# Kernel tuning notes

Hardware: AMD Instinct MI355X
Metric: run time of the kernel (lower is better)

Reference implementation:

```python
import jax, jax.numpy as jnp
import numpy as np

POSE, Z, H, E = 62, 32, 256, 6

def setup_inputs() -> dict:
    key = jax.random.key(0)
    ks = jax.random.split(key, 32)
    it = iter(ks)
    def W(o, i):
        return (jax.random.normal(next(it), (o, i), jnp.float32) * 0.05)
    def B(o):
        return jnp.zeros((o,), jnp.float32)
    def WE(o, i):
        return (jax.random.normal(next(it), (E, o, i), jnp.float32) * 0.05)
    def BE(o):
        return jnp.zeros((E, o), jnp.float32)
    d = {}
    d['prev_pose'] = jax.random.normal(next(it), (POSE,), jnp.float32)
    d['curr_pose'] = jax.random.normal(next(it), (POSE,), jnp.float32)
    d['eps'] = jax.random.normal(next(it), (Z,), jnp.float32)
    # encoder
    d['enc_w0'], d['enc_b0'] = W(H, POSE + POSE), B(H)
    d['enc_w1'], d['enc_b1'] = W(H, H), B(H)
    d['enc_w2'], d['enc_b2'] = W(H, H), B(H)
    d['mu_w'], d['mu_b'] = W(Z, H), B(Z)
    d['lv_w'], d['lv_b'] = W(Z, H), B(Z)
    # gating network
    d['gate_w0'], d['gate_b0'] = W(H, Z + POSE), B(H)
    d['gate_w1'], d['gate_b1'] = W(H, H), B(H)
    d['gate_w2'], d['gate_b2'] = W(H, H), B(H)
    d['gate_w3'], d['gate_b3'] = W(E, H), B(E)
    # 6 experts, stacked on leading expert axis
    d['exp_w0'], d['exp_b0'] = WE(H, Z + POSE), BE(H)
    d['exp_w1'], d['exp_b1'] = WE(H, Z + H), BE(H)
    d['exp_w2'], d['exp_b2'] = WE(H, Z + H), BE(H)
    d['exp_w3'], d['exp_b3'] = WE(POSE, Z + H), BE(POSE)
    return d

def _forward(prev_pose, curr_pose, eps,
             enc_w0, enc_b0, enc_w1, enc_b1, enc_w2, enc_b2,
             mu_w, mu_b, lv_w, lv_b,
             gate_w0, gate_b0, gate_w1, gate_b1, gate_w2, gate_b2,
             gate_w3, gate_b3,
             exp_w0, exp_b0, exp_w1, exp_b1, exp_w2, exp_b2,
             exp_w3, exp_b3):
    elu = jax.nn.elu
    # encode
    x = elu(enc_w0 @ jnp.concatenate([prev_pose, curr_pose]) + enc_b0)
    x = elu(enc_w1 @ x + enc_b1)
    x = elu(enc_w2 @ x + enc_b2)
    mu = mu_w @ x + mu_b
    logvar = lv_w @ x + lv_b
    # reparameterize (eps supplied as input for determinism)
    z = mu + eps * jnp.exp(0.5 * logvar)
    # gating network (raw logits, no softmax -- as in the original)
    g_in = jnp.concatenate([z, prev_pose])  # [94]
    g = elu(gate_w0 @ g_in + gate_b0)
    g = elu(gate_w1 @ g + gate_b1)
    g = elu(gate_w2 @ g + gate_b2)
    gates = gate_w3 @ g + gate_b3  # [6]
    # all 6 experts batched along leading axis e
    z_e = jnp.broadcast_to(z, (E, Z))  # [6,32]
    h = elu(jnp.einsum('eoh,h->eo', exp_w0, g_in) + exp_b0)       # [6,256]
    h = elu(jnp.einsum('eoh,eh->eo', exp_w1,
                       jnp.concatenate([z_e, h], axis=1)) + exp_b1)
    h = elu(jnp.einsum('eoh,eh->eo', exp_w2,
                       jnp.concatenate([z_e, h], axis=1)) + exp_b2)
    out_e = jnp.einsum('eoh,eh->eo', exp_w3,
                       jnp.concatenate([z_e, h], axis=1)) + exp_b3  # [6,62]
    decoded = jnp.sum(out_e * gates[:, None], axis=0)  # [62]
    return decoded, mu, logvar

def reference(prev_pose, curr_pose, eps,
              enc_w0, enc_b0, enc_w1, enc_b1, enc_w2, enc_b2,
              mu_w, mu_b, lv_w, lv_b,
              gate_w0, gate_b0, gate_w1, gate_b1, gate_w2, gate_b2,
              gate_w3, gate_b3,
              exp_w0, exp_b0, exp_w1, exp_b1, exp_w2, exp_b2,
              exp_w3, exp_b3):
    return _forward(prev_pose, curr_pose, eps,
                    enc_w0, enc_b0, enc_w1, enc_b1, enc_w2, enc_b2,
                    mu_w, mu_b, lv_w, lv_b,
                    gate_w0, gate_b0, gate_w1, gate_b1, gate_w2, gate_b2,
                    gate_w3, gate_b3,
                    exp_w0, exp_b0, exp_w1, exp_b1, exp_w2, exp_b2,
                    exp_w3, exp_b3)
```

## Files before the change

kernel.cpp:

```cpp
#include <hip/hip_runtime.h>
#include <math.h>


#define NWG   256
#define BLOCK 256

__device__ __align__(128) float g_a0[256];
__device__ __align__(128) float g_a1[256];
__device__ __align__(128) float g_a2[256];
__device__ __align__(128) float g_mu[32];
__device__ __align__(128) float g_lv[32];
__device__ __align__(128) float g_g0[256];
__device__ __align__(128) float g_g1[256];
__device__ __align__(128) float g_g2[256];
__device__ __align__(128) float g_gates[32];
__device__ __align__(128) float g_h0[1536];
__device__ __align__(128) float g_h1[1536];
__device__ __align__(128) float g_h2[1536];
__device__ __align__(128) float g_oute[384];

struct P {
  const float *prev, *curr, *eps;
  const float *ew0,*eb0,*ew1,*eb1,*ew2,*eb2;
  const float *muw,*mub,*lvw,*lvb;
  const float *gw0,*gb0,*gw1,*gb1,*gw2,*gb2,*gw3,*gb3;
  const float *xw0,*xb0,*xw1,*xb1,*xw2,*xb2,*xw3,*xb3;
  float* out;
};

__device__ __forceinline__ float cload(const float* a) {
  int v = __hip_atomic_load((const int*)a, __ATOMIC_RELAXED,
                            __HIP_MEMORY_SCOPE_AGENT);
  return __int_as_float(v);
}
__device__ __forceinline__ void cstore(float* a, float v) {
  __hip_atomic_store((int*)a, __float_as_int(v), __ATOMIC_RELAXED,
                     __HIP_MEMORY_SCOPE_AGENT);
}
__device__ __forceinline__ float4 cload4(const float* a) {
  float4 r;
  r.x = cload(a + 0); r.y = cload(a + 1);
  r.z = cload(a + 2); r.w = cload(a + 3);
  return r;
}
__device__ __forceinline__ float wred(float v) {
#pragma unroll
  for (int m = 32; m; m >>= 1) v += __shfl_xor(v, m, 64);
  return v;
}
__device__ __forceinline__ float elu(float x) { return x > 0.f ? x : expm1f(x); }
__device__ __forceinline__ float dot4(float4 a, float4 b) {
  return a.x*b.x + a.y*b.y + a.z*b.z + a.w*b.w;
}

__device__ __forceinline__ void gridbar(int* flags, int phase) {
  __syncthreads();
  if (threadIdx.x == 0)
    __hip_atomic_store(&flags[blockIdx.x * 16], phase,
                       __ATOMIC_RELAXED, __HIP_MEMORY_SCOPE_AGENT);
  if (threadIdx.x < 64) {
    const int l = threadIdx.x;
    for (;;) {
      int v0 = __hip_atomic_load(&flags[(l)       * 16], __ATOMIC_RELAXED, __HIP_MEMORY_SCOPE_AGENT);
      int v1 = __hip_atomic_load(&flags[(l +  64) * 16], __ATOMIC_RELAXED, __HIP_MEMORY_SCOPE_AGENT);
      int v2 = __hip_atomic_load(&flags[(l + 128) * 16], __ATOMIC_RELAXED, __HIP_MEMORY_SCOPE_AGENT);
      int v3 = __hip_atomic_load(&flags[(l + 192) * 16], __ATOMIC_RELAXED, __HIP_MEMORY_SCOPE_AGENT);
      if (min(min(v0, v1), min(v2, v3)) >= phase) break;
      __builtin_amdgcn_s_sleep(2);
    }
  }
  __syncthreads();
}

__device__ __forceinline__ void row288(const float* wr, float b,
                                       float4 z4, const float* hsrc,
                                       float* dst, bool doelu, int lane) {
  float4 w = *(const float4*)(wr + 4 * lane);
  float we = (lane < 32) ? wr[256 + lane] : 0.f;
  float4 xh = z4;
  if (lane >= 8) xh = cload4(hsrc + 4 * lane - 32);
  float s = dot4(w, xh);
  if (lane < 32) s += we * cload(hsrc + 224 + lane);
  s = wred(s);
  if (!lane) cstore(dst, doelu ? elu(s + b) : (s + b));
}

__device__ __forceinline__ void row256(const float* wr, float b,
                                       const float* xsrc, float* dst,
                                       bool doelu, int lane) {
  float4 w = *(const float4*)(wr + 4 * lane);
  float4 x = cload4(xsrc + 4 * lane);
  float s = wred(dot4(w, x));
  if (!lane) cstore(dst, doelu ? elu(s + b) : (s + b));
}

__global__ __launch_bounds__(BLOCK, 1) void mvae_main(P p, int* flags) {
  const int tid  = threadIdx.x;
  const int lane = tid & 63;
  const int wvin = tid >> 6;
  const int Wv   = blockIdx.x * 4 + wvin;

  __shared__ float s_o[384];
  __shared__ float s_gg[8];

  if (Wv < 256) {
    const float* wr = p.ew0 + Wv * 124;
    float wa = wr[lane];
    float wb = (lane < 60) ? wr[64 + lane] : 0.f;
    float xa = (lane < 62) ? p.prev[lane] : p.curr[lane - 62];
    float xb = (lane < 60) ? p.curr[lane + 2] : 0.f;
    float s = wred(wa * xa + wb * xb);
    if (!lane) cstore(&g_a0[Wv], elu(s + p.eb0[Wv]));
  }
  gridbar(flags, 1);

  if (Wv < 256)
    row256(p.ew1 + Wv * 256, p.eb1[Wv], g_a0, &g_a1[Wv], true, lane);
  gridbar(flags, 2);

  if (Wv < 256)
    row256(p.ew2 + Wv * 256, p.eb2[Wv], g_a1, &g_a2[Wv], true, lane);
  gridbar(flags, 3);

  if (Wv < 64) {
    const float* wr = (Wv < 32) ? p.muw + Wv * 256 : p.lvw + (Wv - 32) * 256;
    float4 w = *(const float4*)(wr + 4 * lane);
    float4 x = cload4(g_a2 + 4 * lane);
    float s = wred(dot4(w, x));
    if (!lane) {
      if (Wv < 32) { float v = s + p.mub[Wv]; cstore(&g_mu[Wv], v); p.out[62 + Wv] = v; }
      else { int r = Wv - 32; float v = s + p.lvb[r]; cstore(&g_lv[r], v); p.out[94 + r] = v; }
    }
  }
  gridbar(flags, 4);

  float zs = 0.f;
  if (lane < 32)
    zs = cload(&g_mu[lane]) + p.eps[lane] * expf(0.5f * cload(&g_lv[lane]));
  float4 z4;
  z4.x = __shfl(zs, (4 * lane + 0) & 63, 64);
  z4.y = __shfl(zs, (4 * lane + 1) & 63, 64);
  z4.z = __shfl(zs, (4 * lane + 2) & 63, 64);
  z4.w = __shfl(zs, (4 * lane + 3) & 63, 64);
  float prevA = (lane >= 32 && lane < 94) ? p.prev[lane - 32] : 0.f;
  float prevB = (lane < 30) ? p.prev[32 + lane] : 0.f;
  float xa94 = (lane < 32) ? zs : prevA;

  {
#pragma unroll
    for (int k = 0; k < 2; ++k) {
      int r = Wv + 1024 * k;
      if (r < 1792) {
        const float* wr = (r < 256) ? p.gw0 + r * 94 : p.xw0 + (size_t)(r - 256) * 94;
        float wa = wr[lane];
        float wb = (lane < 30) ? wr[64 + lane] : 0.f;
        float s = wred(wa * xa94 + wb * prevB);
        if (!lane) {
          if (r < 256) cstore(&g_g0[r], elu(s + p.gb0[r]));
          else         cstore(&g_h0[r - 256], elu(s + p.xb0[r - 256]));
        }
      }
    }
  }
  gridbar(flags, 5);

  {
#pragma unroll
    for (int k = 0; k < 2; ++k) {
      int r = Wv + 1024 * k;
      if (r < 1792) {
        if (r < 256)
          row256(p.gw1 + r * 256, p.gb1[r], g_g0, &g_g1[r], true, lane);
        else {
          int q = r - 256, e = q >> 8;
          row288(p.xw1 + (size_t)q * 288, p.xb1[q], z4, g_h0 + e * 256,
                 &g_h1[q], true, lane);
        }
      }
    }
  }
  gridbar(flags, 6);

  {
#pragma unroll
    for (int k = 0; k < 2; ++k) {
      int r = Wv + 1024 * k;
      if (r < 1792) {
        if (r < 256)
          row256(p.gw2 + r * 256, p.gb2[r], g_g1, &g_g2[r], true, lane);
        else {
          int q = r - 256, e = q >> 8;
          row288(p.xw2 + (size_t)q * 288, p.xb2[q], z4, g_h1 + e * 256,
                 &g_h2[q], true, lane);
        }
      }
    }
  }
  gridbar(flags, 7);

  if (Wv < 6) {
    row256(p.gw3 + Wv * 256, p.gb3[Wv], g_g2, &g_gates[Wv], false, lane);
  } else if (Wv < 378) {
    int q = Wv - 6, e = q / 62;
    row288(p.xw3 + (size_t)q * 288, p.xb3[q], z4, g_h2 + e * 256,
           &g_oute[q], false, lane);
  }
  gridbar(flags, 8);

  if (blockIdx.x == 0) {
    s_o[tid] = cload(&g_oute[tid]);
    if (tid < 116) s_o[tid + 256] = cload(&g_oute[tid + 256]);
    if (tid < 6)   s_gg[tid] = cload(&g_gates[tid]);
    __syncthreads();
    if (tid < 62) {
      float s = 0.f;
#pragma unroll
      for (int e = 0; e < 6; ++e) s += s_o[e * 62 + tid] * s_gg[e];
      p.out[tid] = s;
    }
  }
}

extern "C" void kernel_launch(void* const* d_in, const int* in_sizes, int n_in,
                              void* d_out, int out_size, void* d_ws, size_t ws_size,
                              hipStream_t stream) {
  (void)in_sizes; (void)n_in; (void)out_size; (void)ws_size;
  const float* const* in = (const float* const*)d_in;
  P p;
  p.prev = in[0];  p.curr = in[1];  p.eps = in[2];
  p.ew0 = in[3];   p.eb0 = in[4];   p.ew1 = in[5];  p.eb1 = in[6];
  p.ew2 = in[7];   p.eb2 = in[8];
  p.muw = in[9];   p.mub = in[10];  p.lvw = in[11]; p.lvb = in[12];
  p.gw0 = in[13];  p.gb0 = in[14];  p.gw1 = in[15]; p.gb1 = in[16];
  p.gw2 = in[17];  p.gb2 = in[18];  p.gw3 = in[19]; p.gb3 = in[20];
  p.xw0 = in[21];  p.xb0 = in[22];  p.xw1 = in[23]; p.xb1 = in[24];
  p.xw2 = in[25];  p.xb2 = in[26];  p.xw3 = in[27]; p.xb3 = in[28];
  p.out = (float*)d_out;

  int* flags = (int*)d_ws;
  hipMemsetAsync(flags, 0, NWG * 16 * sizeof(int), stream);
  mvae_main<<<NWG, BLOCK, 0, stream>>>(p, flags);
}
```

Before: 35.27 us.

## Prefetch all layer weights into LDS upfront and use self-resetting per-phase barriers

Result: faster. 32.66 us, median of 2 (-7.4%).

```diff
diff --git a/kernel.cpp b/kernel.cpp
--- a/kernel.cpp
+++ b/kernel.cpp
@@ -4,6 +4,7 @@
 
 #define NWG   256
 #define BLOCK 256
+#define MAGIC 0x7E57A11E
 
 __device__ __align__(128) float g_a0[256];
 __device__ __align__(128) float g_a1[256];
@@ -43,6 +44,16 @@
   r.z = cload(a + 2); r.w = cload(a + 3);
   return r;
 }
+__device__ __forceinline__ void gll16(const void* g, void* l) {
+  __builtin_amdgcn_global_load_lds((const __attribute__((address_space(1))) void*)g,
+                                   (__attribute__((address_space(3))) void*)l,
+                                   16, 0, 0);
+}
+__device__ __forceinline__ void gll4(const void* g, void* l) {
+  __builtin_amdgcn_global_load_lds((const __attribute__((address_space(1))) void*)g,
+                                   (__attribute__((address_space(3))) void*)l,
+                                   4, 0, 0);
+}
 __device__ __forceinline__ float wred(float v) {
 #pragma unroll
   for (int m = 32; m; m >>= 1) v += __shfl_xor(v, m, 64);
@@ -53,45 +64,32 @@
   return a.x*b.x + a.y*b.y + a.z*b.z + a.w*b.w;
 }
 
-__device__ __forceinline__ void gridbar(int* flags, int phase) {
+__device__ __forceinline__ int* slotp(int* flags, int ph, int wg) {
+  return &flags[((ph - 1) * NWG + wg) * 16];
+}
+__device__ __forceinline__ void bar_arrive(int* flags, int ph) {
   __syncthreads();
   if (threadIdx.x == 0)
-    __hip_atomic_store(&flags[blockIdx.x * 16], phase,
+    __hip_atomic_store(slotp(flags, ph, blockIdx.x), MAGIC,
                        __ATOMIC_RELAXED, __HIP_MEMORY_SCOPE_AGENT);
+}
+__device__ __forceinline__ void bar_poll(int* flags, int ph) {
   if (threadIdx.x < 64) {
     const int l = threadIdx.x;
     for (;;) {
-      int v0 = __hip_atomic_load(&flags[(l)       * 16], __ATOMIC_RELAXED, __HIP_MEMORY_SCOPE_AGENT);
-      int v1 = __hip_atomic_load(&flags[(l +  64) * 16], __ATOMIC_RELAXED, __HIP_MEMORY_SCOPE_AGENT);
-      int v2 = __hip_atomic_load(&flags[(l + 128) * 16], __ATOMIC_RELAXED, __HIP_MEMORY_SCOPE_AGENT);
-      int v3 = __hip_atomic_load(&flags[(l + 192) * 16], __ATOMIC_RELAXED, __HIP_MEMORY_SCOPE_AGENT);
-      if (min(min(v0, v1), min(v2, v3)) >= phase) break;
+      int v0 = __hip_atomic_load(slotp(flags, ph, l),       __ATOMIC_RELAXED, __HIP_MEMORY_SCOPE_AGENT);
+      int v1 = __hip_atomic_load(slotp(flags, ph, l +  64), __ATOMIC_RELAXED, __HIP_MEMORY_SCOPE_AGENT);
+      int v2 = __hip_atomic_load(slotp(flags, ph, l + 128), __ATOMIC_RELAXED, __HIP_MEMORY_SCOPE_AGENT);
+      int v3 = __hip_atomic_load(slotp(flags, ph, l + 192), __ATOMIC_RELAXED, __HIP_MEMORY_SCOPE_AGENT);
+      if (v0 == MAGIC && v1 == MAGIC && v2 == MAGIC && v3 == MAGIC) break;
       __builtin_amdgcn_s_sleep(2);
     }
   }
   __syncthreads();
 }
-
-__device__ __forceinline__ void row288(const float* wr, float b,
-                                       float4 z4, const float* hsrc,
-                                       float* dst, bool doelu, int lane) {
-  float4 w = *(const float4*)(wr + 4 * lane);
-  float we = (lane < 32) ? wr[256 + lane] : 0.f;
-  float4 xh = z4;
-  if (lane >= 8) xh = cload4(hsrc + 4 * lane - 32);
-  float s = dot4(w, xh);
-  if (lane < 32) s += we * cload(hsrc + 224 + lane);
-  s = wred(s);
-  if (!lane) cstore(dst, doelu ? elu(s + b) : (s + b));
-}
-
-__device__ __forceinline__ void row256(const float* wr, float b,
-                                       const float* xsrc, float* dst,
-                                       bool doelu, int lane) {
-  float4 w = *(const float4*)(wr + 4 * lane);
-  float4 x = cload4(xsrc + 4 * lane);
-  float s = wred(dot4(w, x));
-  if (!lane) cstore(dst, doelu ? elu(s + b) : (s + b));
+__device__ __forceinline__ void gridbar(int* flags, int ph) {
+  bar_arrive(flags, ph);
+  bar_poll(flags, ph);
 }
 
 __global__ __launch_bounds__(BLOCK, 1) void mvae_main(P p, int* flags) {
@@ -100,8 +98,69 @@
   const int wvin = tid >> 6;
   const int Wv   = blockIdx.x * 4 + wvin;
 
+  __shared__ __align__(16) float s_w1[4][256];
+  __shared__ __align__(16) float s_w2[4][256];
+  __shared__ __align__(16) float s_w3[4][256];
+  __shared__ __align__(16) float s_w4[4][2][96];
+  __shared__ __align__(16) float s_w5[4][2][288];
+  __shared__ __align__(16) float s_w6[4][2][288];
+  __shared__ __align__(16) float s_w7[4][288];
   __shared__ float s_o[384];
   __shared__ float s_gg[8];
+
+  if (Wv < 256) {
+    gll16(p.ew1 + Wv * 256 + lane * 4, s_w1[wvin]);
+    gll16(p.ew2 + Wv * 256 + lane * 4, s_w2[wvin]);
+  }
+  if (Wv < 64) {
+    const float* src = (Wv < 32) ? p.muw + Wv * 256 : p.lvw + (Wv - 32) * 256;
+    gll16(src + lane * 4, s_w3[wvin]);
+  }
+#pragma unroll
+  for (int k = 0; k < 2; ++k) {
+    int r = Wv + 1024 * k;
+    if (r < 1792) {
+      const float* src = (r < 256) ? p.gw0 + r * 94 : p.xw0 + (size_t)(r - 256) * 94;
+      float* dst = s_w4[wvin][k];
+      if (lane < 23)       gll16(src + lane * 4, dst);
+      else if (lane == 23) { gll4(src + 92, dst + 69);
+                             gll4(src + 93, dst + 70); }
+    }
+  }
+#pragma unroll
+  for (int k = 0; k < 2; ++k) {
+    int r = Wv + 1024 * k;
+    if (r < 1792) {
+      float* dst = s_w5[wvin][k];
+      if (r < 256) gll16(p.gw1 + r * 256 + lane * 4, dst);
+      else {
+        const float* src = p.xw1 + (size_t)(r - 256) * 288;
+        gll16(src + lane * 4, dst);
+        if (lane < 8) gll16(src + 256 + lane * 4, dst + 256);
+      }
+    }
+  }
+#pragma unroll
+  for (int k = 0; k < 2; ++k) {
+    int r = Wv + 1024 * k;
+    if (r < 1792) {
+      float* dst = s_w6[wvin][k];
+      if (r < 256) gll16(p.gw2 + r * 256 + lane * 4, dst);
+      else {
+        const float* src = p.xw2 + (size_t)(r - 256) * 288;
+        gll16(src + lane * 4, dst);
+        if (lane < 8) gll16(src + 256 + lane * 4, dst + 256);
+      }
+    }
+  }
+  if (Wv < 6) {
+    gll16(p.gw3 + Wv * 256 + lane * 4, s_w7[wvin]);
+  } else if (Wv < 378) {
+    const float* src = p.xw3 + (size_t)(Wv - 6) * 288;
+    float* dst = s_w7[wvin];
+    gll16(src + lane * 4, dst);
+    if (lane < 8) gll16(src + 256 + lane * 4, dst + 256);
+  }
 
   if (Wv < 256) {
     const float* wr = p.ew0 + Wv * 124;
@@ -114,17 +173,24 @@
   }
   gridbar(flags, 1);
 
-  if (Wv < 256)
-    row256(p.ew1 + Wv * 256, p.eb1[Wv], g_a0, &g_a1[Wv], true, lane);
+  if (Wv < 256) {
+    float4 w = *(const float4*)(s_w1[wvin] + 4 * lane);
+    float4 x = cload4(g_a0 + 4 * lane);
+    float s = wred(dot4(w, x));
+    if (!lane) cstore(&g_a1[Wv], elu(s + p.eb1[Wv]));
+  }
   gridbar(flags, 2);
 
-  if (Wv < 256)
-    row256(p.ew2 + Wv * 256, p.eb2[Wv], g_a1, &g_a2[Wv], true, lane);
+  if (Wv < 256) {
+    float4 w = *(const float4*)(s_w2[wvin] + 4 * lane);
+    float4 x = cload4(g_a1 + 4 * lane);
+    float s = wred(dot4(w, x));
+    if (!lane) cstore(&g_a2[Wv], elu(s + p.eb2[Wv]));
+  }
   gridbar(flags, 3);
 
   if (Wv < 64) {
-    const float* wr = (Wv < 32) ? p.muw + Wv * 256 : p.lvw + (Wv - 32) * 256;
-    float4 w = *(const float4*)(wr + 4 * lane);
+    float4 w = *(const float4*)(s_w3[wvin] + 4 * lane);
     float4 x = cload4(g_a2 + 4 * lane);
     float s = wred(dot4(w, x));
     if (!lane) {
@@ -146,79 +212,107 @@
   float prevB = (lane < 30) ? p.prev[32 + lane] : 0.f;
   float xa94 = (lane < 32) ? zs : prevA;
 
-  {
-#pragma unroll
-    for (int k = 0; k < 2; ++k) {
-      int r = Wv + 1024 * k;
-      if (r < 1792) {
-        const float* wr = (r < 256) ? p.gw0 + r * 94 : p.xw0 + (size_t)(r - 256) * 94;
-        float wa = wr[lane];
-        float wb = (lane < 30) ? wr[64 + lane] : 0.f;
-        float s = wred(wa * xa94 + wb * prevB);
-        if (!lane) {
-          if (r < 256) cstore(&g_g0[r], elu(s + p.gb0[r]));
-          else         cstore(&g_h0[r - 256], elu(s + p.xb0[r - 256]));
-        }
+#pragma unroll
+  for (int k = 0; k < 2; ++k) {
+    int r = Wv + 1024 * k;
+    if (r < 1792) {
+      const float* wrow = s_w4[wvin][k];
+      float wa = wrow[lane];
+      float wb = (lane < 30) ? wrow[64 + lane] : 0.f;
+      float s = wred(wa * xa94 + wb * prevB);
+      if (!lane) {
+        if (r < 256) cstore(&g_g0[r], elu(s + p.gb0[r]));
+        else         cstore(&g_h0[r - 256], elu(s + p.xb0[r - 256]));
       }
     }
   }
   gridbar(flags, 5);
 
-  {
-#pragma unroll
-    for (int k = 0; k < 2; ++k) {
-      int r = Wv + 1024 * k;
-      if (r < 1792) {
-        if (r < 256)
-          row256(p.gw1 + r * 256, p.gb1[r], g_g0, &g_g1[r], true, lane);
-        else {
-          int q = r - 256, e = q >> 8;
-          row288(p.xw1 + (size_t)q * 288, p.xb1[q], z4, g_h0 + e * 256,
-                 &g_h1[q], true, lane);
-        }
+#pragma unroll
+  for (int k = 0; k < 2; ++k) {
+    int r = Wv + 1024 * k;
+    if (r < 1792) {
+      const float* wrow = s_w5[wvin][k];
+      float4 w = *(const float4*)(wrow + 4 * lane);
+      if (r < 256) {
+        float4 x = cload4(g_g0 + 4 * lane);
+        float s = wred(dot4(w, x));
+        if (!lane) cstore(&g_g1[r], elu(s + p.gb1[r]));
+      } else {
+        int q = r - 256, e = q >> 8;
+        const float* hsrc = g_h0 + e * 256;
+        float4 xh = z4;
+        if (lane >= 8) xh = cload4(hsrc + 4 * lane - 32);
+        float s = dot4(w, xh);
+        if (lane < 32) s += wrow[256 + lane] * cload(hsrc + 224 + lane);
+        s = wred(s);
+        if (!lane) cstore(&g_h1[q], elu(s + p.xb1[q]));
       }
     }
   }
   gridbar(flags, 6);
 
-  {
-#pragma unroll
-    for (int k = 0; k < 2; ++k) {
-      int r = Wv + 1024 * k;
-      if (r < 1792) {
-        if (r < 256)
-          row256(p.gw2 + r * 256, p.gb2[r], g_g1, &g_g2[r], true, lane);
-        else {
-          int q = r - 256, e = q >> 8;
-          row288(p.xw2 + (size_t)q * 288, p.xb2[q], z4, g_h1 + e * 256,
-                 &g_h2[q], true, lane);
-        }
+#pragma unroll
+  for (int k = 0; k < 2; ++k) {
+    int r = Wv + 1024 * k;
+    if (r < 1792) {
+      const float* wrow = s_w6[wvin][k];
+      float4 w = *(const float4*)(wrow + 4 * lane);
+      if (r < 256) {
+        float4 x = cload4(g_g1 + 4 * lane);
+        float s = wred(dot4(w, x));
+        if (!lane) cstore(&g_g2[r], elu(s + p.gb2[r]));
+      } else {
+        int q = r - 256, e = q >> 8;
+        const float* hsrc = g_h1 + e * 256;
+        float4 xh = z4;
+        if (lane >= 8) xh = cload4(hsrc + 4 * lane - 32);
+        float s = dot4(w, xh);
+        if (lane < 32) s += wrow[256 + lane] * cload(hsrc + 224 + lane);
+        s = wred(s);
+        if (!lane) cstore(&g_h2[q], elu(s + p.xb2[q]));
       }
     }
   }
   gridbar(flags, 7);
 
   if (Wv < 6) {
-    row256(p.gw3 + Wv * 256, p.gb3[Wv], g_g2, &g_gates[Wv], false, lane);
+    float4 w = *(const float4*)(s_w7[wvin] + 4 * lane);
+    float4 x = cload4(g_g2 + 4 * lane);
+    float s = wred(dot4(w, x));
+    if (!lane) cstore(&g_gates[Wv], s + p.gb3[Wv]);
   } else if (Wv < 378) {
     int q = Wv - 6, e = q / 62;
-    row288(p.xw3 + (size_t)q * 288, p.xb3[q], z4, g_h2 + e * 256,
-           &g_oute[q], false, lane);
-  }
-  gridbar(flags, 8);
-
-  if (blockIdx.x == 0) {
-    s_o[tid] = cload(&g_oute[tid]);
-    if (tid < 116) s_o[tid + 256] = cload(&g_oute[tid + 256]);
-    if (tid < 6)   s_gg[tid] = cload(&g_gates[tid]);
-    __syncthreads();
-    if (tid < 62) {
-      float s = 0.f;
-#pragma unroll
-      for (int e = 0; e < 6; ++e) s += s_o[e * 62 + tid] * s_gg[e];
-      p.out[tid] = s;
-    }
-  }
+    const float* wrow = s_w7[wvin];
+    float4 w = *(const float4*)(wrow + 4 * lane);
+    const float* hsrc = g_h2 + e * 256;
+    float4 xh = z4;
+    if (lane >= 8) xh = cload4(hsrc + 4 * lane - 32);
+    float s = dot4(w, xh);
+    if (lane < 32) s += wrow[256 + lane] * cload(hsrc + 224 + lane);
+    s = wred(s);
+    if (!lane) cstore(&g_oute[q], s + p.xb3[q]);
+  }
+
+  bar_arrive(flags, 8);
+  if (blockIdx.x != 0) return;
+  bar_poll(flags, 8);
+
+  s_o[tid] = cload(&g_oute[tid]);
+  if (tid < 116) s_o[tid + 256] = cload(&g_oute[tid + 256]);
+  if (tid < 6)   s_gg[tid] = cload(&g_gates[tid]);
+  __syncthreads();
+  if (tid < 62) {
+    float s = 0.f;
+#pragma unroll
+    for (int e = 0; e < 6; ++e) s += s_o[e * 62 + tid] * s_gg[e];
+    p.out[tid] = s;
+  }
+
+#pragma unroll
+  for (int ph = 1; ph <= 8; ++ph)
+    __hip_atomic_store(slotp(flags, ph, tid), 0,
+                       __ATOMIC_RELAXED, __HIP_MEMORY_SCOPE_AGENT);
 }
 
 extern "C" void kernel_launch(void* const* d_in, const int* in_sizes, int n_in,
@@ -238,6 +332,5 @@
   p.out = (float*)d_out;
 
   int* flags = (int*)d_ws;
-  hipMemsetAsync(flags, 0, NWG * 16 * sizeof(int), stream);
   mvae_main<<<NWG, BLOCK, 0, stream>>>(p, flags);
 }
```
